# Kernel optimization log

Hardware: AMD Instinct MI355X
Metric: run time of the kernel (lower is better)

Reference implementation:

```python
import jax, jax.numpy as jnp
import numpy as np

H = 8  # num_heads, fixed in the module


def setup_inputs() -> dict:
    key = jax.random.key(0)
    ks = jax.random.split(key, 26)
    C = 256          # hidden_dim
    K = 16           # num_corners
    B = 8            # images
    P = 64           # proposals per image
    N = B * P        # total proposals
    Hf = Wf = 14     # feature map HxW (T = 196 keys per proposal)
    Hq = Wq = 10     # query grid (S = 100 queries)
    s = 1.0 / np.sqrt(C)

    def w(k, shape):
        return jax.random.normal(k, shape, jnp.float32) * s

    return {
        "features": jax.random.normal(ks[0], (N, C, Hf, Wf), jnp.float32),
        "query_features": jax.random.normal(ks[1], (B, C, Hq, Wq), jnp.float32),
        # self-attention params (torch MHA: y = x @ W.T + b)
        "wq_s": w(ks[2], (C, C)), "wk_s": w(ks[3], (C, C)), "wv_s": w(ks[4], (C, C)),
        "bq_s": jnp.zeros((C,), jnp.float32), "bk_s": jnp.zeros((C,), jnp.float32), "bv_s": jnp.zeros((C,), jnp.float32),
        "wo_s": w(ks[5], (C, C)), "bo_s": jnp.zeros((C,), jnp.float32),
        # cross-attention params
        "wq_c": w(ks[6], (C, C)), "wk_c": w(ks[7], (C, C)), "wv_c": w(ks[8], (C, C)),
        "bq_c": jnp.zeros((C,), jnp.float32), "bk_c": jnp.zeros((C,), jnp.float32), "bv_c": jnp.zeros((C,), jnp.float32),
        "wo_c": w(ks[9], (C, C)), "bo_c": jnp.zeros((C,), jnp.float32),
        # polygon MLP head
        "w1": w(ks[10], (C, C)), "b1": jnp.zeros((C,), jnp.float32),
        "w2": w(ks[11], (2 * K, C)), "b2": jnp.zeros((2 * K,), jnp.float32),
        # score head
        "ws": w(ks[12], (1, C)), "bs": jnp.zeros((1,), jnp.float32),
    }


def _forward(features, query_features,
             wq_s, wk_s, wv_s, bq_s, bk_s, bv_s, wo_s, bo_s,
             wq_c, wk_c, wv_c, bq_c, bk_c, bv_c, wo_c, bo_c,
             w1, b1, w2, b2, ws, bs):
    B, C = query_features.shape[0], query_features.shape[1]
    dh = C // H
    scale = 1.0 / jnp.sqrt(jnp.asarray(dh, jnp.float32))

    # query_features: (B,C,Hq,Wq) -> (S,B,C)
    qf = query_features.reshape(B, C, -1).transpose(2, 0, 1)
    S = qf.shape[0]

    # ---- self-attention over queries ----
    q = (qf @ wq_s.T + bq_s).reshape(S, B, H, dh)
    k = (qf @ wk_s.T + bk_s).reshape(S, B, H, dh)
    v = (qf @ wv_s.T + bv_s).reshape(S, B, H, dh)
    att = jax.nn.softmax(jnp.einsum('sbhd,tbhd->bhst', q, k) * scale, axis=-1)
    qsa = jnp.einsum('bhst,tbhd->sbhd', att, v).reshape(S, B, C) @ wo_s.T + bo_s  # (S,B,C)

    # features: (N,C,Hf,Wf) -> (B,P,T,C) with T=Hf*Wf, P=N//B
    N = features.shape[0]
    P = N // B
    feats = features.reshape(N, C, -1).transpose(0, 2, 1).reshape(B, P, -1, C)

    # ---- cross-attention: same (S,C) query broadcast over P proposals ----
    qc = (qsa @ wq_c.T + bq_c).reshape(S, B, H, dh)
    kc = (feats @ wk_c.T + bk_c).reshape(B, P, -1, H, dh)
    vc = (feats @ wv_c.T + bv_c).reshape(B, P, -1, H, dh)
    sc = jnp.einsum('sbhd,bpthd->bphst', qc, kc) * scale  # (B,P,H,S,T)
    a = jax.nn.softmax(sc, axis=-1)
    o = jnp.einsum('bphst,bpthd->bpshd', a, vc).reshape(B, P, S, C) @ wo_c.T + bo_c  # (B,P,S,C)

    # ---- heads, then mean over the S query positions ----
    h1 = jax.nn.relu(o @ w1.T + b1)
    polygons = (h1 @ w2.T + b2).mean(axis=2).reshape(N, -1)          # (N, 2K)
    scores = jax.nn.sigmoid(o @ ws.T + bs).mean(axis=2).reshape(N, 1)  # (N, 1)
    return polygons, scores


def reference(features, query_features,
              wq_s, wk_s, wv_s, bq_s, bk_s, bv_s, wo_s, bo_s,
              wq_c, wk_c, wv_c, bq_c, bk_c, bv_c, wo_c, bo_c,
              w1, b1, w2, b2, ws, bs):
    return _forward(features, query_features,
                    wq_s, wk_s, wv_s, bq_s, bk_s, bv_s, wo_s, bo_s,
                    wq_c, wk_c, wv_c, bq_c, bk_c, bv_c, wo_c, bo_c,
                    w1, b1, w2, b2, ws, bs)
```

## Files before the change

### kernel.cpp

```cpp
#include <hip/hip_runtime.h>
#include <hip/hip_bf16.h>


typedef __attribute__((ext_vector_type(8))) short bf16x8;
typedef __attribute__((ext_vector_type(4))) float f32x4;

__device__ __forceinline__ float bf2f(ushort u) {
    union { float f; uint u32; } v; v.u32 = ((uint)u) << 16; return v.f;
}
__device__ __forceinline__ ushort f2bf(float f) {
    union { float f; uint u; } v; v.f = f;
    uint r = v.u + 0x7FFF + ((v.u >> 16) & 1);
    return (ushort)(r >> 16);
}
__device__ __forceinline__ f32x4 MFMA(bf16x8 a, bf16x8 b, f32x4 c) {
    return __builtin_amdgcn_mfma_f32_16x16x32_bf16(a, b, c, 0, 0, 0);
}

#define SCALE_DH 0.17677669529663687f

#define TOTALW (2337 * 256)
#define QCPN   (8 * 8 * 112 * 32)
#define NBIAS  2337

__global__ void prep_kernel(const float* w0, const float* w1_, const float* w2_,
                            const float* w3, const float* w4, const float* w5,
                            const float* w6, const float* w7, const float* w8,
                            const float* w9, const float* w10,
                            const float* b0, const float* b1_, const float* b2_,
                            const float* b3, const float* b4, const float* b5,
                            const float* b6, const float* b7, const float* b8,
                            const float* b9, const float* b10,
                            ushort* wbf, float* bias, ushort* qcp)
{
    for (size_t i = blockIdx.x * blockDim.x + threadIdx.x;
         i < (size_t)TOTALW + QCPN + NBIAS; i += (size_t)gridDim.x * blockDim.x) {
        if (i < TOTALW) {
            int row = (int)(i >> 8), col = (int)(i & 255);
            const float* sp; int base;
            if      (row < 256)  { sp = w0;  base = 0; }
            else if (row < 512)  { sp = w1_; base = 256; }
            else if (row < 768)  { sp = w2_; base = 512; }
            else if (row < 1024) { sp = w3;  base = 768; }
            else if (row < 1280) { sp = w4;  base = 1024; }
            else if (row < 1536) { sp = w5;  base = 1280; }
            else if (row < 1792) { sp = w6;  base = 1536; }
            else if (row < 2048) { sp = w7;  base = 1792; }
            else if (row < 2304) { sp = w8;  base = 2048; }
            else if (row < 2336) { sp = w9;  base = 2304; }
            else                 { sp = w10; base = 2336; }
            wbf[i] = f2bf(sp[(size_t)(row - base) * 256 + col]);
        } else if (i < (size_t)TOTALW + QCPN) {
            qcp[i - TOTALW] = 0;
        } else {
            int idx = (int)(i - TOTALW - QCPN);
            const float* sp; int base;
            if      (idx < 256)  { sp = b0;  base = 0; }
            else if (idx < 512)  { sp = b1_; base = 256; }
            else if (idx < 768)  { sp = b2_; base = 512; }
            else if (idx < 1024) { sp = b3;  base = 768; }
            else if (idx < 1280) { sp = b4;  base = 1024; }
            else if (idx < 1536) { sp = b5;  base = 1280; }
            else if (idx < 1792) { sp = b6;  base = 1536; }
            else if (idx < 2048) { sp = b7;  base = 1792; }
            else if (idx < 2304) { sp = b8;  base = 2048; }
            else if (idx < 2336) { sp = b9;  base = 2304; }
            else                 { sp = b10; base = 2336; }
            bias[idx] = sp[idx - base];
        }
    }
}

template<int ASRC, int GS, int EPI>
__global__ __launch_bounds__(256)
void gemm_rows(const void* Aptr, const ushort* Wall, const float* Ball,
               ushort* Out, int M, int Wrow0, int Brow0, int ldo)
{
    __shared__ ushort As[64 * 40];
    __shared__ ushort Bs[128 * 40];
    int tid = threadIdx.x;
    int lane = tid & 63, w = tid >> 6;
    int lr = lane & 15, lg = lane >> 4;
    int r0 = blockIdx.x * 64;
    int j0 = blockIdx.y * 128;

    f32x4 acc[4][2];
    #pragma unroll
    for (int mt = 0; mt < 4; ++mt)
        #pragma unroll
        for (int nt = 0; nt < 2; ++nt) { f32x4 z = {0.f,0.f,0.f,0.f}; acc[mt][nt] = z; }

    for (int ks = 0; ks < 8; ++ks) {
        int c0 = ks * 32;
        {
            int i = tid >> 2, q = tid & 3;
            int r = r0 + i;
            if (ASRC == 0) {
                uint4 v = make_uint4(0u,0u,0u,0u);
                if (r < M) v = *(const uint4*)((const ushort*)Aptr + (size_t)r * 256 + c0 + q * 8);
                *(uint4*)(&As[i * 40 + q * 8]) = v;
            } else {
                uint u[4] = {0u,0u,0u,0u};
                if (r < M) {
                    int g = r / GS, o = r - g * GS;
                    const float* src = (const float*)Aptr + (size_t)g * 256 * GS + o;
                    #pragma unroll
                    for (int k2 = 0; k2 < 4; ++k2) {
                        ushort a0 = f2bf(src[(size_t)(c0 + q * 8 + 2 * k2)     * GS]);
                        ushort a1 = f2bf(src[(size_t)(c0 + q * 8 + 2 * k2 + 1) * GS]);
                        u[k2] = (uint)a0 | ((uint)a1 << 16);
                    }
                }
                *(uint4*)(&As[i * 40 + q * 8]) = make_uint4(u[0], u[1], u[2], u[3]);
            }
        }
        {
            int jj = tid >> 1, half = tid & 1;
            const ushort* src = Wall + (size_t)(Wrow0 + j0 + jj) * 256 + c0 + half * 16;
            ushort* dst = &Bs[jj * 40 + half * 16];
            *(uint4*)(dst)     = *(const uint4*)(src);
            *(uint4*)(dst + 8) = *(const uint4*)(src + 8);
        }
        __syncthreads();
        bf16x8 bfr[2];
        #pragma unroll
        for (int nt = 0; nt < 2; ++nt)
            bfr[nt] = *(const bf16x8*)(&Bs[(w * 32 + nt * 16 + lr) * 40 + lg * 8]);
        #pragma unroll
        for (int mt = 0; mt < 4; ++mt) {
            bf16x8 afr = *(const bf16x8*)(&As[(mt * 16 + lr) * 40 + lg * 8]);
            acc[mt][0] = MFMA(afr, bfr[0], acc[mt][0]);
            acc[mt][1] = MFMA(afr, bfr[1], acc[mt][1]);
        }
        __syncthreads();
    }
    #pragma unroll
    for (int mt = 0; mt < 4; ++mt) {
        #pragma unroll
        for (int nt = 0; nt < 2; ++nt) {
            int jc = j0 + w * 32 + nt * 16 + lr;
            float bias = Ball[Brow0 + jc];
            #pragma unroll
            for (int rg = 0; rg < 4; ++rg) {
                int r = r0 + mt * 16 + lg * 4 + rg;
                if (r >= M) continue;
                float vv = acc[mt][nt][rg] + bias;
                if (EPI == 0) {
                    Out[(size_t)r * ldo + jc] = f2bf(vv);
                } else {
                    int b = r / 100, s = r - b * 100;
                    int h = jc >> 5, d = jc & 31;
                    Out[(((size_t)(b * 8 + h)) * 112 + s) * 32 + d] = f2bf(vv * SCALE_DH);
                }
            }
        }
    }
}

__global__ __launch_bounds__(128)
void self_attn(const ushort* qkv, ushort* sav)
{
    __shared__ float kls[100][33];
    __shared__ float vls[100][33];
    __shared__ float sls[100][101];
    int bh = blockIdx.x; int b = bh >> 3, h = bh & 7;
    int tid = threadIdx.x;
    for (int idx = tid; idx < 100 * 32; idx += 128) {
        int t = idx >> 5, d = idx & 31;
        kls[t][d] = bf2f(qkv[((size_t)(b * 100 + t)) * 768 + 256 + h * 32 + d]);
        vls[t][d] = bf2f(qkv[((size_t)(b * 100 + t)) * 768 + 512 + h * 32 + d]);
    }
    __syncthreads();
    if (tid < 100) {
        int s = tid;
        float q[32];
        #pragma unroll
        for (int d = 0; d < 32; ++d)
            q[d] = bf2f(qkv[((size_t)(b * 100 + s)) * 768 + h * 32 + d]) * SCALE_DH;
        float mx = -1e30f;
        for (int t = 0; t < 100; ++t) {
            float sc = 0.f;
            #pragma unroll
            for (int d = 0; d < 32; ++d) sc += q[d] * kls[t][d];
            sls[s][t] = sc; mx = fmaxf(mx, sc);
        }
        float sum = 0.f;
        for (int t = 0; t < 100; ++t) {
            float p = __expf(sls[s][t] - mx);
            sls[s][t] = p; sum += p;
        }
        float inv = 1.f / sum;
        float acc2[32];
        #pragma unroll
        for (int d = 0; d < 32; ++d) acc2[d] = 0.f;
        for (int t = 0; t < 100; ++t) {
            float pv = sls[s][t];
            #pragma unroll
            for (int d = 0; d < 32; ++d) acc2[d] += pv * vls[t][d];
        }
        #pragma unroll
        for (int d = 0; d < 32; ++d)
            sav[((size_t)(b * 100 + s)) * 256 + h * 32 + d] = f2bf(acc2[d] * inv);
    }
}

__global__ __launch_bounds__(512, 2)
void kvproj(const float* features, const ushort* Wall, const float* Ball,
            ushort* kc, ushort* vc, int n_base)
{
    __shared__ ushort featT[224 * 264];
    int tid = threadIdx.x;
    int lane = tid & 63, w = tid >> 6;
    int lr = lane & 15, lg = lane >> 4;
    int nl = blockIdx.x;
    int n  = n_base + nl;
    const float* fb = features + (size_t)n * 256 * 196;

    bf16x8 wf[4][8];
    #pragma unroll
    for (int ct = 0; ct < 4; ++ct) {
        int wrow = ((ct < 2) ? 1280 : 1536) + w * 32 + (ct & 1) * 16;
        #pragma unroll
        for (int ks = 0; ks < 8; ++ks)
            wf[ct][ks] = *(const bf16x8*)(Wall + (size_t)(wrow + lr) * 256 + ks * 32 + lg * 8);
    }
    float biask0 = Ball[1280 + w * 32 + lr];
    float biask1 = Ball[1296 + w * 32 + lr];
    float biasv0 = Ball[1536 + w * 32 + lr];
    float biasv1 = Ball[1552 + w * 32 + lr];

    for (int it = 0; it < 25; ++it) {
        int g = tid + it * 512;
        if (g < 12544) {
            int c = g / 49, tq = g - c * 49;
            float4 v = *(const float4*)(fb + (size_t)c * 196 + tq * 4);
            float vv[4] = {v.x, v.y, v.z, v.w};
            #pragma unroll
            for (int i = 0; i < 4; ++i) {
                int j = (i + tq) & 3;
                featT[(tq * 4 + j) * 264 + c] = f2bf(vv[j]);
            }
        }
    }
    for (int idx = tid; idx < 28 * 264; idx += 512)
        featT[196 * 264 + idx] = 0;
    __syncthreads();

    for (int tt = 0; tt < 14; ++tt) {
        bf16x8 af[8];
        #pragma unroll
        for (int ks = 0; ks < 8; ++ks)
            af[ks] = *(const bf16x8*)(&featT[(tt * 16 + lr) * 264 + ks * 32 + lg * 8]);
        f32x4 acc[4];
        #pragma unroll
        for (int ct = 0; ct < 4; ++ct) { f32x4 z = {0.f,0.f,0.f,0.f}; acc[ct] = z; }
        #pragma unroll
        for (int ks = 0; ks < 8; ++ks)
            #pragma unroll
            for (int ct = 0; ct < 4; ++ct)
                acc[ct] = MFMA(af[ks], wf[ct][ks], acc[ct]);

        int tb = tt * 16 + lg * 4;
        #pragma unroll
        for (int rg = 0; rg < 4; ++rg) {
            kc[((size_t)nl * 224 + tb + rg) * 256 + w * 32 + lr]      = f2bf(acc[0][rg] + biask0);
            kc[((size_t)nl * 224 + tb + rg) * 256 + w * 32 + 16 + lr] = f2bf(acc[1][rg] + biask1);
        }
        size_t vb0 = ((size_t)nl * 256 + w * 32 + lr) * 224 + tb;
        size_t vb1 = ((size_t)nl * 256 + w * 32 + 16 + lr) * 224 + tb;
        uint a01 = (uint)f2bf(acc[2][0] + biasv0) | ((uint)f2bf(acc[2][1] + biasv0) << 16);
        uint a23 = (uint)f2bf(acc[2][2] + biasv0) | ((uint)f2bf(acc[2][3] + biasv0) << 16);
        uint b01 = (uint)f2bf(acc[3][0] + biasv1) | ((uint)f2bf(acc[3][1] + biasv1) << 16);
        uint b23 = (uint)f2bf(acc[3][2] + biasv1) | ((uint)f2bf(acc[3][3] + biasv1) << 16);
        *(uint*)(vc + vb0)     = a01;
        *(uint*)(vc + vb0 + 2) = a23;
        *(uint*)(vc + vb1)     = b01;
        *(uint*)(vc + vb1 + 2) = b23;
    }
}

__global__ __launch_bounds__(512)
void attn_fuse(const ushort* qcp, const ushort* kc, const ushort* vc,
               const ushort* Wall, const float* Ball, float* outp, int n_base)
{
    __shared__ char smem[130816];
    ushort* P   = (ushort*)smem;
    ushort* KCs = (ushort*)(smem + 71680);
    ushort* VCs = (ushort*)(smem + 88576);
    ushort* OL  = (ushort*)smem;
    ushort* O2  = (ushort*)(smem + 71680);
    float* hbar = (float*)(smem + 59392);
    float* scb  = (float*)(smem + 60416);

    int tid = threadIdx.x;
    int lane = tid & 63; int w = tid >> 6;
    int lr = lane & 15, lg = lane >> 4;
    int nl = blockIdx.x; int n = n_base + nl;
    int b = n >> 6;
    const ushort* kcn = kc + (size_t)nl * 224 * 256;
    const ushort* vcn = vc + (size_t)nl * 256 * 224;

    bf16x8 qf[7];
    #pragma unroll
    for (int mt = 0; mt < 7; ++mt)
        qf[mt] = *(const bf16x8*)(qcp + ((((size_t)(b * 8 + w)) * 112 + mt * 16 + lr) * 32 + lg * 8));

    bf16x8 ones;
    #pragma unroll
    for (int j = 0; j < 8; ++j) ones[j] = (short)0x3F80;

    f32x4 o_acc[7][2], l_acc[7];
    #pragma unroll
    for (int mt = 0; mt < 7; ++mt) {
        f32x4 z = {0.f,0.f,0.f,0.f};
        o_acc[mt][0] = z; o_acc[mt][1] = z; l_acc[mt] = z;
    }

    int kt = tid >> 4, kseg = tid & 15;
    int vcc = tid >> 1, vhalf = tid & 1;
    uint4 kr0, kr1, vr0, vr1;
    {
        const ushort* s  = kcn + (size_t)kt * 256 + kseg * 16;
        const ushort* s2 = vcn + (size_t)vcc * 224 + vhalf * 16;
        kr0 = *(const uint4*)(s);  kr1 = *(const uint4*)(s + 8);
        vr0 = *(const uint4*)(s2); vr1 = *(const uint4*)(s2 + 8);
    }

    for (int ch = 0; ch < 7; ++ch) {
        int t0 = ch * 32;
        __syncthreads();
        {
            ushort* d  = &KCs[kt * 264 + kseg * 16];
            ushort* d2 = &VCs[vcc * 40 + vhalf * 16];
            *(uint4*)(d)      = kr0; *(uint4*)(d + 8)  = kr1;
            *(uint4*)(d2)     = vr0; *(uint4*)(d2 + 8) = vr1;
        }
        __syncthreads();
        if (ch < 6) {
            int t0n = t0 + 32;
            const ushort* s  = kcn + ((size_t)(t0n + kt)) * 256 + kseg * 16;
            const ushort* s2 = vcn + (size_t)vcc * 224 + t0n + vhalf * 16;
            kr0 = *(const uint4*)(s);  kr1 = *(const uint4*)(s + 8);
            vr0 = *(const uint4*)(s2); vr1 = *(const uint4*)(s2 + 8);
        }

        bf16x8 bk[2];
        #pragma unroll
        for (int nt = 0; nt < 2; ++nt)
            bk[nt] = *(const bf16x8*)(&KCs[(nt * 16 + lr) * 264 + w * 32 + lg * 8]);
        bool mask0 = (t0 + lr)      >= 196;
        bool mask1 = (t0 + 16 + lr) >= 196;
        #pragma unroll
        for (int mt = 0; mt < 7; ++mt) {
            f32x4 z = {0.f,0.f,0.f,0.f};
            f32x4 s0v = MFMA(qf[mt], bk[0], z);
            f32x4 s1v = MFMA(qf[mt], bk[1], z);
            #pragma unroll
            for (int r = 0; r < 4; ++r) {
                float p0 = mask0 ? 0.f : __expf(s0v[r]);
                float p1 = mask1 ? 0.f : __expf(s1v[r]);
                int srow = mt * 16 + lg * 4 + r;
                P[(w * 112 + srow) * 40 + lr]      = f2bf(p0);
                P[(w * 112 + srow) * 40 + 16 + lr] = f2bf(p1);
            }
        }
        bf16x8 bv[2];
        #pragma unroll
        for (int nt = 0; nt < 2; ++nt)
            bv[nt] = *(const bf16x8*)(&VCs[(w * 32 + nt * 16 + lr) * 40 + lg * 8]);
        #pragma unroll
        for (int mt = 0; mt < 7; ++mt) {
            bf16x8 pf = *(const bf16x8*)(&P[(w * 112 + mt * 16 + lr) * 40 + lg * 8]);
            o_acc[mt][0] = MFMA(pf, bv[0], o_acc[mt][0]);
            o_acc[mt][1] = MFMA(pf, bv[1], o_acc[mt][1]);
            l_acc[mt]    = MFMA(pf, ones,  l_acc[mt]);
        }
    }

    __syncthreads();
    #pragma unroll
    for (int mt = 0; mt < 7; ++mt) {
        #pragma unroll
        for (int r = 0; r < 4; ++r) {
            float inv = 1.f / l_acc[mt][r];
            int srow = mt * 16 + lg * 4 + r;
            OL[srow * 264 + w * 32 + lr]      = f2bf(o_acc[mt][0][r] * inv);
            OL[srow * 264 + w * 32 + 16 + lr] = f2bf(o_acc[mt][1][r] * inv);
        }
    }
    __syncthreads();

    {
        f32x4 a2[7][2];
        #pragma unroll
        for (int mt = 0; mt < 7; ++mt)
            #pragma unroll
            for (int nt = 0; nt < 2; ++nt) { f32x4 z = {0.f,0.f,0.f,0.f}; a2[mt][nt] = z; }
        for (int ks = 0; ks < 8; ++ks) {
            int c0 = ks * 32;
            bf16x8 bw[2];
            #pragma unroll
            for (int nt = 0; nt < 2; ++nt)
                bw[nt] = *(const bf16x8*)(Wall + (size_t)(1792 + w * 32 + nt * 16 + lr) * 256 + c0 + lg * 8);
            #pragma unroll
            for (int mt = 0; mt < 7; ++mt) {
                bf16x8 af = *(const bf16x8*)(&OL[(mt * 16 + lr) * 264 + c0 + lg * 8]);
                a2[mt][0] = MFMA(af, bw[0], a2[mt][0]);
                a2[mt][1] = MFMA(af, bw[1], a2[mt][1]);
            }
        }
        #pragma unroll
        for (int mt = 0; mt < 7; ++mt)
            #pragma unroll
            for (int nt = 0; nt < 2; ++nt) {
                float bias = Ball[1792 + w * 32 + nt * 16 + lr];
                #pragma unroll
                for (int r = 0; r < 4; ++r) {
                    int srow = mt * 16 + lg * 4 + r;
                    O2[srow * 264 + w * 32 + nt * 16 + lr] = f2bf(a2[mt][nt][r] + bias);
                }
            }
    }
    __syncthreads();

    {
        f32x4 a2[7][2];
        #pragma unroll
        for (int mt = 0; mt < 7; ++mt)
            #pragma unroll
            for (int nt = 0; nt < 2; ++nt) { f32x4 z = {0.f,0.f,0.f,0.f}; a2[mt][nt] = z; }
        for (int ks = 0; ks < 8; ++ks) {
            int c0 = ks * 32;
            bf16x8 bw[2];
            #pragma unroll
            for (int nt = 0; nt < 2; ++nt)
                bw[nt] = *(const bf16x8*)(Wall + (size_t)(2048 + w * 32 + nt * 16 + lr) * 256 + c0 + lg * 8);
            #pragma unroll
            for (int mt = 0; mt < 7; ++mt) {
                bf16x8 af = *(const bf16x8*)(&O2[(mt * 16 + lr) * 264 + c0 + lg * 8]);
                a2[mt][0] = MFMA(af, bw[0], a2[mt][0]);
                a2[mt][1] = MFMA(af, bw[1], a2[mt][1]);
            }
        }
        __syncthreads();
        #pragma unroll
        for (int mt = 0; mt < 7; ++mt)
            #pragma unroll
            for (int nt = 0; nt < 2; ++nt) {
                float bias = Ball[2048 + w * 32 + nt * 16 + lr];
                #pragma unroll
                for (int r = 0; r < 4; ++r) {
                    int srow = mt * 16 + lg * 4 + r;
                    float v = a2[mt][nt][r] + bias;
                    v = v > 0.f ? v : 0.f;
                    OL[srow * 264 + w * 32 + nt * 16 + lr] = f2bf(v);
                }
            }
    }
    __syncthreads();

    if (tid < 256) {
        float s = 0.f;
        for (int srow = 0; srow < 100; ++srow) s += bf2f(OL[srow * 264 + tid]);
        hbar[tid] = s * 0.01f;
    }
    if (tid < 100) {
        float s = 0.f;
        for (int c2 = 0; c2 < 256; ++c2)
            s += bf2f(O2[tid * 264 + c2]) * bf2f(Wall[(size_t)2336 * 256 + c2]);
        s += Ball[2336];
        scb[tid] = 1.f / (1.f + __expf(-s));
    }
    __syncthreads();
    if (tid < 32) {
        float s = 0.f;
        for (int c2 = 0; c2 < 256; ++c2)
            s += hbar[c2] * bf2f(Wall[(size_t)(2304 + tid) * 256 + c2]);
        s += Ball[2304 + tid];
        outp[(size_t)n * 32 + tid] = s;
    }
    if (tid == 64) {
        float s = 0.f;
        for (int i2 = 0; i2 < 100; ++i2) s += scb[i2];
        outp[16384 + n] = s * 0.01f;
    }
}

extern "C" void kernel_launch(void* const* d_in, const int* in_sizes, int n_in,
                              void* d_out, int out_size, void* d_ws, size_t ws_size,
                              hipStream_t stream)
{
    const float* features = (const float*)d_in[0];
    const float* qfeat    = (const float*)d_in[1];
    char* ws = (char*)d_ws;

    ushort* wbf  = (ushort*)ws;
    float*  bias = (float*)(ws + 1196544);
    ushort* qkv  = (ushort*)(ws + 1206016);
    ushort* sav  = (ushort*)(ws + 2434816);
    ushort* osb  = (ushort*)(ws + 2844416);
    ushort* qcp  = (ushort*)(ws + 3254016);
    ushort* kvb  = (ushort*)(ws + 3712768);

    prep_kernel<<<dim3(512), dim3(256), 0, stream>>>(
        (const float*)d_in[2], (const float*)d_in[3], (const float*)d_in[4],
        (const float*)d_in[8], (const float*)d_in[10], (const float*)d_in[11],
        (const float*)d_in[12], (const float*)d_in[16], (const float*)d_in[18],
        (const float*)d_in[20], (const float*)d_in[22],
        (const float*)d_in[5], (const float*)d_in[6], (const float*)d_in[7],
        (const float*)d_in[9], (const float*)d_in[13], (const float*)d_in[14],
        (const float*)d_in[15], (const float*)d_in[17], (const float*)d_in[19],
        (const float*)d_in[21], (const float*)d_in[23],
        wbf, bias, qcp);

    gemm_rows<1, 100, 0><<<dim3(13, 6), dim3(256), 0, stream>>>(
        qfeat, wbf, bias, qkv, 800, 0, 0, 768);
    self_attn<<<dim3(64), dim3(128), 0, stream>>>(qkv, sav);
    gemm_rows<0, 1, 0><<<dim3(13, 2), dim3(256), 0, stream>>>(
        sav, wbf, bias, osb, 800, 768, 768, 256);
    gemm_rows<0, 1, 1><<<dim3(13, 2), dim3(256), 0, stream>>>(
        osb, wbf, bias, qcp, 800, 1024, 1024, 0);

    const size_t per_n = 229376;
    long avail = (long)ws_size - 3712768L;
    int Np = 512;
    if (avail < (long)(per_n * 512)) {
        Np = (int)(avail / (long)per_n);
        if (Np < 1) Np = 1;
    }
    ushort* kcb = kvb;
    ushort* vcb = kvb + (size_t)Np * 224 * 256;
    float* outp = (float*)d_out;
    for (int n0 = 0; n0 < 512; n0 += Np) {
        int cnt = (512 - n0 < Np) ? (512 - n0) : Np;
        kvproj<<<dim3(cnt), dim3(512), 0, stream>>>(features, wbf, bias, kcb, vcb, n0);
        attn_fuse<<<dim3(cnt), dim3(512), 0, stream>>>(qcp, kcb, vcb, wbf, bias, outp, n0);
    }
}
```

Before: 230.4 us.

## Fuse K/V projection into cross-attention kernel with double-buffered feature staging

Merges the kvproj and attn_fuse kernels into a single fused_cross kernel. Each warp now projects its own head's K and V for every 32-token chunk straight into LDS, so the projected K/V never take a round trip through global memory. The next chunk's features are prefetched into registers and written to a second LDS buffer while the current chunk's attention is computed. The cost is more LDS per block and fewer resident blocks per CU. Q fragments are also reloaded from global memory on every chunk instead of being held in registers.

```diff
diff --git a/kernel.cpp b/kernel.cpp
--- a/kernel.cpp
+++ b/kernel.cpp
@@ -205,105 +205,57 @@
 }
 
 __global__ __launch_bounds__(512, 2)
-void kvproj(const float* features, const ushort* Wall, const float* Ball,
-            ushort* kc, ushort* vc, int n_base)
+void fused_cross(const float* features, const ushort* qcp, const ushort* Wall,
+                 const float* Ball, float* outp)
 {
-    __shared__ ushort featT[224 * 264];
+    __shared__ char smem[119808];
+    ushort* featT0 = (ushort*)smem;
+    ushort* featT1 = (ushort*)(smem + 16896);
+    ushort* Kp  = (ushort*)(smem + 33792);
+    ushort* Vp  = (ushort*)(smem + 54272);
+    ushort* Pp  = (ushort*)(smem + 74752);
+    ushort* OL  = (ushort*)smem;
+    float* hbar = (float*)(smem + 59136);
+    float* scb  = (float*)(smem + 60160);
+    ushort* O2  = (ushort*)(smem + 60608);
+
     int tid = threadIdx.x;
-    int lane = tid & 63, w = tid >> 6;
+    int lane = tid & 63; int w = tid >> 6;
     int lr = lane & 15, lg = lane >> 4;
-    int nl = blockIdx.x;
-    int n  = n_base + nl;
+    int n = blockIdx.x; int b = n >> 6;
     const float* fb = features + (size_t)n * 256 * 196;
+    ushort* Kw = Kp + w * 1280;
+    ushort* Vw = Vp + w * 1280;
+    ushort* Pw = Pp + w * 640;
 
     bf16x8 wf[4][8];
     #pragma unroll
     for (int ct = 0; ct < 4; ++ct) {
-        int wrow = ((ct < 2) ? 1280 : 1536) + w * 32 + (ct & 1) * 16;
+        int wrow = ((ct < 2) ? 1280 : 1536) + w * 32 + (ct & 1) * 16 + lr;
         #pragma unroll
         for (int ks = 0; ks < 8; ++ks)
-            wf[ct][ks] = *(const bf16x8*)(Wall + (size_t)(wrow + lr) * 256 + ks * 32 + lg * 8);
+            wf[ct][ks] = *(const bf16x8*)(Wall + (size_t)wrow * 256 + ks * 32 + lg * 8);
     }
     float biask0 = Ball[1280 + w * 32 + lr];
     float biask1 = Ball[1296 + w * 32 + lr];
     float biasv0 = Ball[1536 + w * 32 + lr];
     float biasv1 = Ball[1552 + w * 32 + lr];
 
-    for (int it = 0; it < 25; ++it) {
-        int g = tid + it * 512;
-        if (g < 12544) {
-            int c = g / 49, tq = g - c * 49;
+    {
+        #pragma unroll
+        for (int i = 0; i < 4; ++i) {
+            int idx = tid + i * 512;
+            int c = idx >> 3, tq = idx & 7;
             float4 v = *(const float4*)(fb + (size_t)c * 196 + tq * 4);
             float vv[4] = {v.x, v.y, v.z, v.w};
             #pragma unroll
-            for (int i = 0; i < 4; ++i) {
-                int j = (i + tq) & 3;
-                featT[(tq * 4 + j) * 264 + c] = f2bf(vv[j]);
-            }
-        }
-    }
-    for (int idx = tid; idx < 28 * 264; idx += 512)
-        featT[196 * 264 + idx] = 0;
+            for (int k = 0; k < 4; ++k) {
+                int j = (k + tq) & 3;
+                featT0[(tq * 4 + j) * 264 + c] = f2bf(vv[j]);
+            }
+        }
+    }
     __syncthreads();
-
-    for (int tt = 0; tt < 14; ++tt) {
-        bf16x8 af[8];
-        #pragma unroll
-        for (int ks = 0; ks < 8; ++ks)
-            af[ks] = *(const bf16x8*)(&featT[(tt * 16 + lr) * 264 + ks * 32 + lg * 8]);
-        f32x4 acc[4];
-        #pragma unroll
-        for (int ct = 0; ct < 4; ++ct) { f32x4 z = {0.f,0.f,0.f,0.f}; acc[ct] = z; }
-        #pragma unroll
-        for (int ks = 0; ks < 8; ++ks)
-            #pragma unroll
-            for (int ct = 0; ct < 4; ++ct)
-                acc[ct] = MFMA(af[ks], wf[ct][ks], acc[ct]);
-
-        int tb = tt * 16 + lg * 4;
-        #pragma unroll
-        for (int rg = 0; rg < 4; ++rg) {
-            kc[((size_t)nl * 224 + tb + rg) * 256 + w * 32 + lr]      = f2bf(acc[0][rg] + biask0);
-            kc[((size_t)nl * 224 + tb + rg) * 256 + w * 32 + 16 + lr] = f2bf(acc[1][rg] + biask1);
-        }
-        size_t vb0 = ((size_t)nl * 256 + w * 32 + lr) * 224 + tb;
-        size_t vb1 = ((size_t)nl * 256 + w * 32 + 16 + lr) * 224 + tb;
-        uint a01 = (uint)f2bf(acc[2][0] + biasv0) | ((uint)f2bf(acc[2][1] + biasv0) << 16);
-        uint a23 = (uint)f2bf(acc[2][2] + biasv0) | ((uint)f2bf(acc[2][3] + biasv0) << 16);
-        uint b01 = (uint)f2bf(acc[3][0] + biasv1) | ((uint)f2bf(acc[3][1] + biasv1) << 16);
-        uint b23 = (uint)f2bf(acc[3][2] + biasv1) | ((uint)f2bf(acc[3][3] + biasv1) << 16);
-        *(uint*)(vc + vb0)     = a01;
-        *(uint*)(vc + vb0 + 2) = a23;
-        *(uint*)(vc + vb1)     = b01;
-        *(uint*)(vc + vb1 + 2) = b23;
-    }
-}
-
-__global__ __launch_bounds__(512)
-void attn_fuse(const ushort* qcp, const ushort* kc, const ushort* vc,
-               const ushort* Wall, const float* Ball, float* outp, int n_base)
-{
-    __shared__ char smem[130816];
-    ushort* P   = (ushort*)smem;
-    ushort* KCs = (ushort*)(smem + 71680);
-    ushort* VCs = (ushort*)(smem + 88576);
-    ushort* OL  = (ushort*)smem;
-    ushort* O2  = (ushort*)(smem + 71680);
-    float* hbar = (float*)(smem + 59392);
-    float* scb  = (float*)(smem + 60416);
-
-    int tid = threadIdx.x;
-    int lane = tid & 63; int w = tid >> 6;
-    int lr = lane & 15, lg = lane >> 4;
-    int nl = blockIdx.x; int n = n_base + nl;
-    int b = n >> 6;
-    const ushort* kcn = kc + (size_t)nl * 224 * 256;
-    const ushort* vcn = vc + (size_t)nl * 256 * 224;
-
-    bf16x8 qf[7];
-    #pragma unroll
-    for (int mt = 0; mt < 7; ++mt)
-        qf[mt] = *(const bf16x8*)(qcp + ((((size_t)(b * 8 + w)) * 112 + mt * 16 + lr) * 32 + lg * 8));
 
     bf16x8 ones;
     #pragma unroll
@@ -316,68 +268,112 @@
         o_acc[mt][0] = z; o_acc[mt][1] = z; l_acc[mt] = z;
     }
 
-    int kt = tid >> 4, kseg = tid & 15;
-    int vcc = tid >> 1, vhalf = tid & 1;
-    uint4 kr0, kr1, vr0, vr1;
-    {
-        const ushort* s  = kcn + (size_t)kt * 256 + kseg * 16;
-        const ushort* s2 = vcn + (size_t)vcc * 224 + vhalf * 16;
-        kr0 = *(const uint4*)(s);  kr1 = *(const uint4*)(s + 8);
-        vr0 = *(const uint4*)(s2); vr1 = *(const uint4*)(s2 + 8);
-    }
-
+    float4 pre[4];
     for (int ch = 0; ch < 7; ++ch) {
+        ushort* Fc = (ch & 1) ? featT1 : featT0;
+        ushort* Fn = (ch & 1) ? featT0 : featT1;
         int t0 = ch * 32;
-        __syncthreads();
+
         {
-            ushort* d  = &KCs[kt * 264 + kseg * 16];
-            ushort* d2 = &VCs[vcc * 40 + vhalf * 16];
-            *(uint4*)(d)      = kr0; *(uint4*)(d + 8)  = kr1;
-            *(uint4*)(d2)     = vr0; *(uint4*)(d2 + 8) = vr1;
-        }
-        __syncthreads();
+            f32x4 aK[2][2];
+            #pragma unroll
+            for (int mt = 0; mt < 2; ++mt)
+                #pragma unroll
+                for (int nt = 0; nt < 2; ++nt) { f32x4 z = {0.f,0.f,0.f,0.f}; aK[mt][nt] = z; }
+            #pragma unroll
+            for (int mt = 0; mt < 2; ++mt)
+                #pragma unroll
+                for (int ks = 0; ks < 8; ++ks) {
+                    bf16x8 af = *(const bf16x8*)(&Fc[(mt * 16 + lr) * 264 + ks * 32 + lg * 8]);
+                    aK[mt][0] = MFMA(af, wf[0][ks], aK[mt][0]);
+                    aK[mt][1] = MFMA(af, wf[1][ks], aK[mt][1]);
+                }
+            #pragma unroll
+            for (int mt = 0; mt < 2; ++mt)
+                #pragma unroll
+                for (int rg = 0; rg < 4; ++rg) {
+                    int tl = mt * 16 + lg * 4 + rg;
+                    Kw[tl * 40 + lr]      = f2bf(aK[mt][0][rg] + biask0);
+                    Kw[tl * 40 + 16 + lr] = f2bf(aK[mt][1][rg] + biask1);
+                }
+        }
+        {
+            f32x4 aV[2][2];
+            #pragma unroll
+            for (int mt = 0; mt < 2; ++mt)
+                #pragma unroll
+                for (int nt = 0; nt < 2; ++nt) { f32x4 z = {0.f,0.f,0.f,0.f}; aV[mt][nt] = z; }
+            #pragma unroll
+            for (int mt = 0; mt < 2; ++mt)
+                #pragma unroll
+                for (int ks = 0; ks < 8; ++ks) {
+                    bf16x8 af = *(const bf16x8*)(&Fc[(mt * 16 + lr) * 264 + ks * 32 + lg * 8]);
+                    aV[mt][0] = MFMA(af, wf[2][ks], aV[mt][0]);
+                    aV[mt][1] = MFMA(af, wf[3][ks], aV[mt][1]);
+                }
+            #pragma unroll
+            for (int mt = 0; mt < 2; ++mt)
+                #pragma unroll
+                for (int nt = 0; nt < 2; ++nt) {
+                    float bv_ = nt ? biasv1 : biasv0;
+                    int tb = mt * 16 + lg * 4;
+                    uint v01 = (uint)f2bf(aV[mt][nt][0] + bv_) | ((uint)f2bf(aV[mt][nt][1] + bv_) << 16);
+                    uint v23 = (uint)f2bf(aV[mt][nt][2] + bv_) | ((uint)f2bf(aV[mt][nt][3] + bv_) << 16);
+                    *(uint*)(Vw + (nt * 16 + lr) * 40 + tb)     = v01;
+                    *(uint*)(Vw + (nt * 16 + lr) * 40 + tb + 2) = v23;
+                }
+        }
         if (ch < 6) {
             int t0n = t0 + 32;
-            const ushort* s  = kcn + ((size_t)(t0n + kt)) * 256 + kseg * 16;
-            const ushort* s2 = vcn + (size_t)vcc * 224 + t0n + vhalf * 16;
-            kr0 = *(const uint4*)(s);  kr1 = *(const uint4*)(s + 8);
-            vr0 = *(const uint4*)(s2); vr1 = *(const uint4*)(s2 + 8);
-        }
-
-        bf16x8 bk[2];
-        #pragma unroll
-        for (int nt = 0; nt < 2; ++nt)
-            bk[nt] = *(const bf16x8*)(&KCs[(nt * 16 + lr) * 264 + w * 32 + lg * 8]);
+            #pragma unroll
+            for (int i = 0; i < 4; ++i) {
+                int idx = tid + i * 512;
+                int c = idx >> 3, tq = idx & 7;
+                int tg = t0n + tq * 4;
+                float4 z = {0.f,0.f,0.f,0.f};
+                pre[i] = (tg < 196) ? *(const float4*)(fb + (size_t)c * 196 + tg) : z;
+            }
+        }
+        bf16x8 bk0 = *(const bf16x8*)(&Kw[lr * 40 + lg * 8]);
+        bf16x8 bk1 = *(const bf16x8*)(&Kw[(16 + lr) * 40 + lg * 8]);
+        bf16x8 bv0 = *(const bf16x8*)(&Vw[lr * 40 + lg * 8]);
+        bf16x8 bv1 = *(const bf16x8*)(&Vw[(16 + lr) * 40 + lg * 8]);
         bool mask0 = (t0 + lr)      >= 196;
         bool mask1 = (t0 + 16 + lr) >= 196;
         #pragma unroll
         for (int mt = 0; mt < 7; ++mt) {
+            bf16x8 qfm = *(const bf16x8*)(qcp + ((((size_t)(b * 8 + w)) * 112 + mt * 16 + lr) * 32 + lg * 8));
             f32x4 z = {0.f,0.f,0.f,0.f};
-            f32x4 s0v = MFMA(qf[mt], bk[0], z);
-            f32x4 s1v = MFMA(qf[mt], bk[1], z);
+            f32x4 s0 = MFMA(qfm, bk0, z);
+            f32x4 s1 = MFMA(qfm, bk1, z);
             #pragma unroll
             for (int r = 0; r < 4; ++r) {
-                float p0 = mask0 ? 0.f : __expf(s0v[r]);
-                float p1 = mask1 ? 0.f : __expf(s1v[r]);
-                int srow = mt * 16 + lg * 4 + r;
-                P[(w * 112 + srow) * 40 + lr]      = f2bf(p0);
-                P[(w * 112 + srow) * 40 + 16 + lr] = f2bf(p1);
-            }
-        }
-        bf16x8 bv[2];
-        #pragma unroll
-        for (int nt = 0; nt < 2; ++nt)
-            bv[nt] = *(const bf16x8*)(&VCs[(w * 32 + nt * 16 + lr) * 40 + lg * 8]);
-        #pragma unroll
-        for (int mt = 0; mt < 7; ++mt) {
-            bf16x8 pf = *(const bf16x8*)(&P[(w * 112 + mt * 16 + lr) * 40 + lg * 8]);
-            o_acc[mt][0] = MFMA(pf, bv[0], o_acc[mt][0]);
-            o_acc[mt][1] = MFMA(pf, bv[1], o_acc[mt][1]);
-            l_acc[mt]    = MFMA(pf, ones,  l_acc[mt]);
-        }
-    }
-
-    __syncthreads();
+                float p0 = mask0 ? 0.f : __expf(s0[r]);
+                float p1 = mask1 ? 0.f : __expf(s1[r]);
+                Pw[(lg * 4 + r) * 40 + lr]      = f2bf(p0);
+                Pw[(lg * 4 + r) * 40 + 16 + lr] = f2bf(p1);
+            }
+            bf16x8 pf = *(const bf16x8*)(&Pw[lr * 40 + lg * 8]);
+            o_acc[mt][0] = MFMA(pf, bv0, o_acc[mt][0]);
+            o_acc[mt][1] = MFMA(pf, bv1, o_acc[mt][1]);
+            l_acc[mt]    = MFMA(pf, ones, l_acc[mt]);
+        }
+        if (ch < 6) {
+            #pragma unroll
+            for (int i = 0; i < 4; ++i) {
+                int idx = tid + i * 512;
+                int c = idx >> 3, tq = idx & 7;
+                float vv[4] = {pre[i].x, pre[i].y, pre[i].z, pre[i].w};
+                #pragma unroll
+                for (int k = 0; k < 4; ++k) {
+                    int j = (k + tq) & 3;
+                    Fn[(tq * 4 + j) * 264 + c] = f2bf(vv[j]);
+                }
+            }
+        }
+        __syncthreads();
+    }
+
     #pragma unroll
     for (int mt = 0; mt < 7; ++mt) {
         #pragma unroll
@@ -500,7 +496,6 @@
     ushort* sav  = (ushort*)(ws + 2434816);
     ushort* osb  = (ushort*)(ws + 2844416);
     ushort* qcp  = (ushort*)(ws + 3254016);
-    ushort* kvb  = (ushort*)(ws + 3712768);
 
     prep_kernel<<<dim3(512), dim3(256), 0, stream>>>(
         (const float*)d_in[2], (const float*)d_in[3], (const float*)d_in[4],
@@ -521,19 +516,6 @@
     gemm_rows<0, 1, 1><<<dim3(13, 2), dim3(256), 0, stream>>>(
         osb, wbf, bias, qcp, 800, 1024, 1024, 0);
 
-    const size_t per_n = 229376;
-    long avail = (long)ws_size - 3712768L;
-    int Np = 512;
-    if (avail < (long)(per_n * 512)) {
-        Np = (int)(avail / (long)per_n);
-        if (Np < 1) Np = 1;
-    }
-    ushort* kcb = kvb;
-    ushort* vcb = kvb + (size_t)Np * 224 * 256;
-    float* outp = (float*)d_out;
-    for (int n0 = 0; n0 < 512; n0 += Np) {
-        int cnt = (512 - n0 < Np) ? (512 - n0) : Np;
-        kvproj<<<dim3(cnt), dim3(512), 0, stream>>>(features, wbf, bias, kcb, vcb, n0);
-        attn_fuse<<<dim3(cnt), dim3(512), 0, stream>>>(qcp, kcb, vcb, wbf, bias, outp, n0);
-    }
-}
+    fused_cross<<<dim3(512), dim3(512), 0, stream>>>(
+        features, qcp, wbf, bias, (float*)d_out);
+}
```

After: 409.0 us. 77.5% more time.

## Split K/V projection over token halves and stream K/V from registers in attention

Applied to the files above, without the earlier changes.

kvproj now runs on a 2D grid, with each block handling 112 tokens. It stages fp32 features in shared memory in two channel halves, converts them to bf16 on the fly, and swaps MFMA operand roles so the weights are the A operand. attn_fuse drops its shared-memory K/V staging and the two block-wide barriers per chunk. Each wave loads its own K/V fragments straight from global memory with register double buffering, and keeps a small per-wave P scratch. The aim is more parallelism in the projection and less synchronisation in attention, at the cost of more global loads and scalar-strided V stores.

```diff
diff --git a/kernel.cpp b/kernel.cpp
--- a/kernel.cpp
+++ b/kernel.cpp
@@ -12,6 +12,10 @@
     union { float f; uint u; } v; v.f = f;
     uint r = v.u + 0x7FFF + ((v.u >> 16) & 1);
     return (ushort)(r >> 16);
+}
+__device__ __forceinline__ uint pk2(float a, float b) {
+    __hip_bfloat162 h = __float22bfloat162_rn(make_float2(a, b));
+    union { __hip_bfloat162 h2; uint u; } c; c.h2 = h; return c.u;
 }
 __device__ __forceinline__ f32x4 MFMA(bf16x8 a, bf16x8 b, f32x4 c) {
     return __builtin_amdgcn_mfma_f32_16x16x32_bf16(a, b, c, 0, 0, 0);
@@ -208,89 +212,95 @@
 void kvproj(const float* features, const ushort* Wall, const float* Ball,
             ushort* kc, ushort* vc, int n_base)
 {
-    __shared__ ushort featT[224 * 264];
+    __shared__ float Fs[128 * 114];
     int tid = threadIdx.x;
     int lane = tid & 63, w = tid >> 6;
     int lr = lane & 15, lg = lane >> 4;
     int nl = blockIdx.x;
     int n  = n_base + nl;
+    int th = blockIdx.y;
+    int t0b = th * 112;
     const float* fb = features + (size_t)n * 256 * 196;
 
-    bf16x8 wf[4][8];
-    #pragma unroll
-    for (int ct = 0; ct < 4; ++ct) {
-        int wrow = ((ct < 2) ? 1280 : 1536) + w * 32 + (ct & 1) * 16;
-        #pragma unroll
-        for (int ks = 0; ks < 8; ++ks)
-            wf[ct][ks] = *(const bf16x8*)(Wall + (size_t)(wrow + lr) * 256 + ks * 32 + lg * 8);
-    }
-    float biask0 = Ball[1280 + w * 32 + lr];
-    float biask1 = Ball[1296 + w * 32 + lr];
-    float biasv0 = Ball[1536 + w * 32 + lr];
-    float biasv1 = Ball[1552 + w * 32 + lr];
-
-    for (int it = 0; it < 25; ++it) {
-        int g = tid + it * 512;
-        if (g < 12544) {
-            int c = g / 49, tq = g - c * 49;
-            float4 v = *(const float4*)(fb + (size_t)c * 196 + tq * 4);
-            float vv[4] = {v.x, v.y, v.z, v.w};
-            #pragma unroll
-            for (int i = 0; i < 4; ++i) {
-                int j = (i + tq) & 3;
-                featT[(tq * 4 + j) * 264 + c] = f2bf(vv[j]);
-            }
-        }
-    }
-    for (int idx = tid; idx < 28 * 264; idx += 512)
-        featT[196 * 264 + idx] = 0;
-    __syncthreads();
-
-    for (int tt = 0; tt < 14; ++tt) {
-        bf16x8 af[8];
-        #pragma unroll
-        for (int ks = 0; ks < 8; ++ks)
-            af[ks] = *(const bf16x8*)(&featT[(tt * 16 + lr) * 264 + ks * 32 + lg * 8]);
-        f32x4 acc[4];
-        #pragma unroll
-        for (int ct = 0; ct < 4; ++ct) { f32x4 z = {0.f,0.f,0.f,0.f}; acc[ct] = z; }
-        #pragma unroll
-        for (int ks = 0; ks < 8; ++ks)
-            #pragma unroll
-            for (int ct = 0; ct < 4; ++ct)
-                acc[ct] = MFMA(af[ks], wf[ct][ks], acc[ct]);
-
-        int tb = tt * 16 + lg * 4;
-        #pragma unroll
-        for (int rg = 0; rg < 4; ++rg) {
-            kc[((size_t)nl * 224 + tb + rg) * 256 + w * 32 + lr]      = f2bf(acc[0][rg] + biask0);
-            kc[((size_t)nl * 224 + tb + rg) * 256 + w * 32 + 16 + lr] = f2bf(acc[1][rg] + biask1);
-        }
-        size_t vb0 = ((size_t)nl * 256 + w * 32 + lr) * 224 + tb;
-        size_t vb1 = ((size_t)nl * 256 + w * 32 + 16 + lr) * 224 + tb;
-        uint a01 = (uint)f2bf(acc[2][0] + biasv0) | ((uint)f2bf(acc[2][1] + biasv0) << 16);
-        uint a23 = (uint)f2bf(acc[2][2] + biasv0) | ((uint)f2bf(acc[2][3] + biasv0) << 16);
-        uint b01 = (uint)f2bf(acc[3][0] + biasv1) | ((uint)f2bf(acc[3][1] + biasv1) << 16);
-        uint b23 = (uint)f2bf(acc[3][2] + biasv1) | ((uint)f2bf(acc[3][3] + biasv1) << 16);
-        *(uint*)(vc + vb0)     = a01;
-        *(uint*)(vc + vb0 + 2) = a23;
-        *(uint*)(vc + vb1)     = b01;
-        *(uint*)(vc + vb1 + 2) = b23;
-    }
-}
-
-__global__ __launch_bounds__(512)
+    f32x4 acc[7][4];
+    #pragma unroll
+    for (int tt = 0; tt < 7; ++tt)
+        #pragma unroll
+        for (int m = 0; m < 4; ++m) { f32x4 z = {0.f,0.f,0.f,0.f}; acc[tt][m] = z; }
+
+    for (int cs = 0; cs < 2; ++cs) {
+        if (cs) __syncthreads();
+        #pragma unroll
+        for (int i = 0; i < 14; ++i) {
+            int idx = i * 512 + tid;
+            int cl = idx / 56, tq = idx - cl * 56;
+            int t = t0b + tq * 2;
+            float2 v = make_float2(0.f, 0.f);
+            if (t < 196) v = *(const float2*)(fb + (size_t)(cs * 128 + cl) * 196 + t);
+            *(float2*)(&Fs[cl * 114 + tq * 2]) = v;
+        }
+        __syncthreads();
+        bf16x8 af[4][4];
+        #pragma unroll
+        for (int m = 0; m < 4; ++m) {
+            int row = ((m < 2) ? 1280 : 1536) + w * 32 + (m & 1) * 16 + lr;
+            #pragma unroll
+            for (int ksl = 0; ksl < 4; ++ksl)
+                af[m][ksl] = *(const bf16x8*)(Wall + (size_t)row * 256 + cs * 128 + ksl * 32 + lg * 8);
+        }
+        #pragma unroll
+        for (int tt = 0; tt < 7; ++tt) {
+            #pragma unroll
+            for (int ksl = 0; ksl < 4; ++ksl) {
+                const float* bp = &Fs[(ksl * 32 + lg * 8) * 114 + tt * 16 + lr];
+                union { uint4 q; bf16x8 v; } bu;
+                bu.q.x = pk2(bp[0],       bp[114]);
+                bu.q.y = pk2(bp[2 * 114], bp[3 * 114]);
+                bu.q.z = pk2(bp[4 * 114], bp[5 * 114]);
+                bu.q.w = pk2(bp[6 * 114], bp[7 * 114]);
+                #pragma unroll
+                for (int m = 0; m < 4; ++m)
+                    acc[tt][m] = MFMA(af[m][ksl], bu.v, acc[tt][m]);
+            }
+        }
+    }
+
+    #pragma unroll
+    for (int tt = 0; tt < 7; ++tt) {
+        int tloc = t0b + tt * 16 + lr;
+        #pragma unroll
+        for (int m = 0; m < 4; ++m) {
+            int cout0 = w * 32 + (m & 1) * 16 + lg * 4;
+            if (m < 2) {
+                float4 bk4 = *(const float4*)(Ball + 1280 + cout0);
+                ushort4 o;
+                o.x = f2bf(acc[tt][m][0] + bk4.x);
+                o.y = f2bf(acc[tt][m][1] + bk4.y);
+                o.z = f2bf(acc[tt][m][2] + bk4.z);
+                o.w = f2bf(acc[tt][m][3] + bk4.w);
+                *(ushort4*)(kc + ((size_t)nl * 224 + tloc) * 256 + cout0) = o;
+            } else {
+                #pragma unroll
+                for (int rg = 0; rg < 4; ++rg) {
+                    int cout = cout0 + rg;
+                    vc[((size_t)nl * 256 + cout) * 224 + tloc] =
+                        f2bf(acc[tt][m][rg] + Ball[1536 + cout]);
+                }
+            }
+        }
+    }
+}
+
+__global__ __launch_bounds__(512, 2)
 void attn_fuse(const ushort* qcp, const ushort* kc, const ushort* vc,
                const ushort* Wall, const float* Ball, float* outp, int n_base)
 {
     __shared__ char smem[130816];
-    ushort* P   = (ushort*)smem;
-    ushort* KCs = (ushort*)(smem + 71680);
-    ushort* VCs = (ushort*)(smem + 88576);
     ushort* OL  = (ushort*)smem;
-    ushort* O2  = (ushort*)(smem + 71680);
     float* hbar = (float*)(smem + 59392);
     float* scb  = (float*)(smem + 60416);
+    ushort* O2  = (ushort*)(smem + 71680);
+    ushort* Pp  = (ushort*)(smem + 71680);
 
     int tid = threadIdx.x;
     int lane = tid & 63; int w = tid >> 6;
@@ -299,6 +309,7 @@
     int b = n >> 6;
     const ushort* kcn = kc + (size_t)nl * 224 * 256;
     const ushort* vcn = vc + (size_t)nl * 256 * 224;
+    ushort* Pw = Pp + w * 640;
 
     bf16x8 qf[7];
     #pragma unroll
@@ -316,65 +327,45 @@
         o_acc[mt][0] = z; o_acc[mt][1] = z; l_acc[mt] = z;
     }
 
-    int kt = tid >> 4, kseg = tid & 15;
-    int vcc = tid >> 1, vhalf = tid & 1;
-    uint4 kr0, kr1, vr0, vr1;
-    {
-        const ushort* s  = kcn + (size_t)kt * 256 + kseg * 16;
-        const ushort* s2 = vcn + (size_t)vcc * 224 + vhalf * 16;
-        kr0 = *(const uint4*)(s);  kr1 = *(const uint4*)(s + 8);
-        vr0 = *(const uint4*)(s2); vr1 = *(const uint4*)(s2 + 8);
-    }
+    const ushort* kbase = kcn + (size_t)lr * 256 + w * 32 + lg * 8;
+    const ushort* vbase = vcn + ((size_t)(w * 32 + lr)) * 224 + lg * 8;
+
+    bf16x8 ck0, ck1, cv0, cv1;
+    ck0 = *(const bf16x8*)(kbase);
+    ck1 = *(const bf16x8*)(kbase + 16 * 256);
+    cv0 = *(const bf16x8*)(vbase);
+    cv1 = *(const bf16x8*)(vbase + 16 * 224);
 
     for (int ch = 0; ch < 7; ++ch) {
         int t0 = ch * 32;
-        __syncthreads();
-        {
-            ushort* d  = &KCs[kt * 264 + kseg * 16];
-            ushort* d2 = &VCs[vcc * 40 + vhalf * 16];
-            *(uint4*)(d)      = kr0; *(uint4*)(d + 8)  = kr1;
-            *(uint4*)(d2)     = vr0; *(uint4*)(d2 + 8) = vr1;
-        }
-        __syncthreads();
+        bf16x8 nk0, nk1, nv0, nv1;
         if (ch < 6) {
             int t0n = t0 + 32;
-            const ushort* s  = kcn + ((size_t)(t0n + kt)) * 256 + kseg * 16;
-            const ushort* s2 = vcn + (size_t)vcc * 224 + t0n + vhalf * 16;
-            kr0 = *(const uint4*)(s);  kr1 = *(const uint4*)(s + 8);
-            vr0 = *(const uint4*)(s2); vr1 = *(const uint4*)(s2 + 8);
-        }
-
-        bf16x8 bk[2];
-        #pragma unroll
-        for (int nt = 0; nt < 2; ++nt)
-            bk[nt] = *(const bf16x8*)(&KCs[(nt * 16 + lr) * 264 + w * 32 + lg * 8]);
+            nk0 = *(const bf16x8*)(kbase + (size_t)t0n * 256);
+            nk1 = *(const bf16x8*)(kbase + (size_t)(t0n + 16) * 256);
+            nv0 = *(const bf16x8*)(vbase + t0n);
+            nv1 = *(const bf16x8*)(vbase + 16 * 224 + t0n);
+        }
         bool mask0 = (t0 + lr)      >= 196;
         bool mask1 = (t0 + 16 + lr) >= 196;
         #pragma unroll
         for (int mt = 0; mt < 7; ++mt) {
             f32x4 z = {0.f,0.f,0.f,0.f};
-            f32x4 s0v = MFMA(qf[mt], bk[0], z);
-            f32x4 s1v = MFMA(qf[mt], bk[1], z);
+            f32x4 s0 = MFMA(qf[mt], ck0, z);
+            f32x4 s1 = MFMA(qf[mt], ck1, z);
             #pragma unroll
             for (int r = 0; r < 4; ++r) {
-                float p0 = mask0 ? 0.f : __expf(s0v[r]);
-                float p1 = mask1 ? 0.f : __expf(s1v[r]);
-                int srow = mt * 16 + lg * 4 + r;
-                P[(w * 112 + srow) * 40 + lr]      = f2bf(p0);
-                P[(w * 112 + srow) * 40 + 16 + lr] = f2bf(p1);
-            }
-        }
-        bf16x8 bv[2];
-        #pragma unroll
-        for (int nt = 0; nt < 2; ++nt)
-            bv[nt] = *(const bf16x8*)(&VCs[(w * 32 + nt * 16 + lr) * 40 + lg * 8]);
-        #pragma unroll
-        for (int mt = 0; mt < 7; ++mt) {
-            bf16x8 pf = *(const bf16x8*)(&P[(w * 112 + mt * 16 + lr) * 40 + lg * 8]);
-            o_acc[mt][0] = MFMA(pf, bv[0], o_acc[mt][0]);
-            o_acc[mt][1] = MFMA(pf, bv[1], o_acc[mt][1]);
-            l_acc[mt]    = MFMA(pf, ones,  l_acc[mt]);
-        }
+                float p0 = mask0 ? 0.f : __expf(s0[r]);
+                float p1 = mask1 ? 0.f : __expf(s1[r]);
+                Pw[(lg * 4 + r) * 40 + lr]      = f2bf(p0);
+                Pw[(lg * 4 + r) * 40 + 16 + lr] = f2bf(p1);
+            }
+            bf16x8 pf = *(const bf16x8*)(&Pw[lr * 40 + lg * 8]);
+            o_acc[mt][0] = MFMA(pf, cv0, o_acc[mt][0]);
+            o_acc[mt][1] = MFMA(pf, cv1, o_acc[mt][1]);
+            l_acc[mt]    = MFMA(pf, ones, l_acc[mt]);
+        }
+        ck0 = nk0; ck1 = nk1; cv0 = nv0; cv1 = nv1;
     }
 
     __syncthreads();
@@ -533,7 +524,7 @@
     float* outp = (float*)d_out;
     for (int n0 = 0; n0 < 512; n0 += Np) {
         int cnt = (512 - n0 < Np) ? (512 - n0) : Np;
-        kvproj<<<dim3(cnt), dim3(512), 0, stream>>>(features, wbf, bias, kcb, vcb, n0);
+        kvproj<<<dim3(cnt, 2), dim3(512), 0, stream>>>(features, wbf, bias, kcb, vcb, n0);
         attn_fuse<<<dim3(cnt), dim3(512), 0, stream>>>(qcp, kcb, vcb, wbf, bias, outp, n0);
     }
 }
```

Result: slower. 369.3 us (+60.3%).
